# Kernel optimization log

Measured on AMD Instinct MI355X. Metric: run time of the kernel, lower is better.

The kernel has to match this reference:

```python
import jax, jax.numpy as jnp
import numpy as np
import math

SIGMA_DATA = 0.5
SIGMA_MIN = 0.002
SIGMA_MAX = 80.0
B = 32768
STATE = 256
ACT = 64
TD = 16
E = 16
H = 256  # moe hidden = gate_dim = output_dim = hidden_dim//4
IN = STATE + ACT + TD  # 336
TOP_K = 4


def mish(x):
    return x * jnp.tanh(jax.nn.softplus(x))


def setup_inputs() -> dict:
    key = jax.random.key(0)
    ks = jax.random.split(key, 20)
    def xavier(k, shape):
        fan_in, fan_out = shape[-2], shape[-1]
        lim = math.sqrt(6.0 / (fan_in + fan_out))
        return jax.random.uniform(k, shape, jnp.float32, -lim, lim)
    inp = {
        "x": jax.random.normal(ks[0], (B, ACT), jnp.float32),
        "sigma": jax.random.uniform(ks[1], (B,), jnp.float32) * (SIGMA_MAX - SIGMA_MIN) + SIGMA_MIN,
        "state": jax.random.normal(ks[2], (B, STATE), jnp.float32),
        # time MLP: Linear(16,32), Mish, Linear(32,16)
        "tW1": xavier(ks[3], (TD, 2 * TD)), "tb1": jnp.zeros((2 * TD,), jnp.float32),
        "tW2": xavier(ks[4], (2 * TD, TD)), "tb2": jnp.zeros((TD,), jnp.float32),
        # gate: Linear(IN, H), ReLU, (dropout eval), Linear(H, E)
        "gW1": xavier(ks[5], (IN, H)), "gb1": jnp.zeros((H,), jnp.float32),
        "gW2": xavier(ks[6], (H, E)), "gb2": jnp.zeros((E,), jnp.float32),
        # 16 stacked expert MLPs: IN->H->H->H with Mish after each Linear
        "eW1": xavier(ks[7], (E, IN, H)), "eb1": jnp.zeros((E, H), jnp.float32),
        "eW2": xavier(ks[8], (E, H, H)), "eb2": jnp.zeros((E, H), jnp.float32),
        "eW3": xavier(ks[9], (E, H, H)), "eb3": jnp.zeros((E, H), jnp.float32),
        # final layer: Linear(H, ACT)
        "fW": xavier(ks[10], (H, ACT)), "fb": jnp.zeros((ACT,), jnp.float32),
    }
    return inp


def reference(x, sigma, state, tW1, tb1, tW2, tb2, gW1, gb1, gW2, gb2,
              eW1, eb1, eW2, eb2, eW3, eb3, fW, fb):
    # --- consistency-model scalings (boundary condition) ---
    c_skip = SIGMA_DATA ** 2 / ((sigma - SIGMA_MIN) ** 2 + SIGMA_DATA ** 2)
    c_out = (sigma - SIGMA_MIN) * SIGMA_DATA * jax.lax.rsqrt(sigma ** 2 + SIGMA_DATA ** 2)
    c_in = jax.lax.rsqrt(sigma ** 2 + SIGMA_DATA ** 2)
    rescaled_t = 1000.0 * 0.25 * jnp.log(sigma + 1e-44)

    x_in = c_in[:, None] * x

    # --- sinusoidal time embedding (dim=16) + time MLP ---
    half = TD // 2
    freqs = jnp.exp(jnp.arange(half, dtype=jnp.float32) * (-math.log(10000.0) / (half - 1)))
    ang = rescaled_t[:, None] * freqs[None, :]           # [B, 8]
    pe = jnp.concatenate([jnp.sin(ang), jnp.cos(ang)], axis=-1)  # [B, 16]
    t = mish(pe @ tW1 + tb1) @ tW2 + tb2                 # [B, 16]

    inp = jnp.concatenate([x_in, t, state], axis=1)      # [B, 336]

    # --- gate (eval mode: dropout off) ---
    g = jax.nn.relu(inp @ gW1 + gb1) @ gW2 + gb2         # [B, E]
    gate_scores = jax.nn.softmax(g, axis=1)
    top_k_scores, top_k_idx = jax.lax.top_k(gate_scores, TOP_K)  # [B, K]

    # --- run ALL experts densely (as the original does) ---
    h = mish(jnp.einsum('bi,eih->beh', inp, eW1) + eb1)  # [B, E, H]
    h = mish(jnp.einsum('beh,ehk->bek', h, eW2) + eb2)
    expert_out = mish(jnp.einsum('beh,eho->beo', h, eW3) + eb3)  # [B, E, H]

    # --- gather top-k, scale by normalized gate scores, combine ---
    sel = jnp.take_along_axis(expert_out, top_k_idx[:, :, None], axis=1)  # [B, K, H]
    scaled = sel * top_k_scores[:, :, None]
    scaled = scaled / (jnp.sum(top_k_scores, axis=1, keepdims=True)[:, :, None] + 1e-9)
    combined = jnp.sum(scaled, axis=1)                   # [B, H]

    # --- auxiliary loss ---
    one_hot = jax.nn.one_hot(top_k_idx, E, dtype=jnp.float32)  # [B, K, E]
    expert_load = jnp.sum(one_hot, axis=(0, 1)) / (x.shape[0] + 1e-9)
    load_balancing_loss = jnp.var(expert_load, ddof=1)   # torch .var() is unbiased
    entropy = -jnp.mean(jnp.sum(gate_scores * jnp.log(gate_scores + 1e-9), axis=1))
    aux_loss = load_balancing_loss + entropy

    model_out = combined @ fW + fb                       # [B, ACT]
    denoised = c_out[:, None] * model_out + c_skip[:, None] * x
    denoised = jnp.clip(denoised, -1.0, 1.0)             # clip_denoised=True
    return denoised, aux_loss
```

## Files before the change

### kernel.cpp

```cpp
#include <hip/hip_runtime.h>
#include <math.h>

#define BN 32768
#define INDP 352
#define HD 256
#define AD 64
#define EN 16
#define TME 32
#define TMG 16
#define STOT (BN * 4)
#define GRID_E 4112
#define CHUNK_E 514

typedef __attribute__((ext_vector_type(8))) short s8v;
typedef __attribute__((ext_vector_type(4))) float f4v;
typedef unsigned short u16;

__device__ __forceinline__ u16 f2bf(float x) {
  unsigned u = __float_as_uint(x);
  return (u16)((u + 0x7fffu + ((u >> 16) & 1u)) >> 16);
}
__device__ __forceinline__ float bf2f(u16 h) { return __uint_as_float(((unsigned)h) << 16); }
__device__ __forceinline__ float rcpf(float a) { float r; asm("v_rcp_f32 %0, %1" : "=v"(r) : "v"(a)); return r; }
__device__ __forceinline__ float mishf(float x) {
  float xc = fminf(x, 30.f);
  float u = __expf(xc);
  float w = fmaf(u, u, u + u);
  return x * w * rcpf(w + 2.f);
}
__device__ __forceinline__ f4v mfma16(s8v a, s8v b, f4v c) {
  return __builtin_amdgcn_mfma_f32_16x16x32_bf16(a, b, c, 0, 0, 0);
}
__device__ __forceinline__ void pack8(const u16* q, u16* d) {
  uint4 u;
  u.x = q[0] | ((unsigned)q[1] << 16); u.y = q[2] | ((unsigned)q[3] << 16);
  u.z = q[4] | ((unsigned)q[5] << 16); u.w = q[6] | ((unsigned)q[7] << 16);
  *(uint4*)d = u;
}

__global__ void k_init(int* __restrict__ counts, int* __restrict__ cursor,
                       float* __restrict__ ent) {
  int i = threadIdx.x;
  if (i < 16) { counts[i] = 0; cursor[i] = 0; }
  if (i == 16) *ent = 0.f;
}

__global__ void k_prep(const float* __restrict__ src, u16* __restrict__ dst,
                       int Ksrc, int Spad, int NT, int N,
                       long sStride, long dStride, int NP, int total) {
  int idx = blockIdx.x * 256 + threadIdx.x;
  if (idx >= total) return;
  int l = idx & 63;
  int t = idx >> 6;
  int nt = t % NT; t /= NT;
  int s = t % Spad; t /= Spad;
  int m = t;
  const float* sp = src + (size_t)m * sStride;
  int n = nt * 16 + (l & 15);
  int kb = s * 32 + (l >> 4) * 8;
  u16 q0[8], q1[8], q2[8];
  #pragma unroll
  for (int i = 0; i < 8; ++i) {
    int k = kb + i;
    float v = (k < Ksrc) ? sp[(size_t)k * N + n] : 0.f;
    u16 a = f2bf(v); float r1 = v - bf2f(a);
    u16 b = f2bf(r1); float r2 = r1 - bf2f(b);
    q0[i] = a; q1[i] = b; q2[i] = f2bf(r2);
  }
  u16* d = dst + (size_t)m * dStride + (size_t)((s * NT + nt) * NP) * 512 + l * 8;
  pack8(q0, d);
  pack8(q1, d + 512);
  if (NP == 3) pack8(q2, d + 1024);
}

__global__ void k_time_inp(const float* __restrict__ x, const float* __restrict__ sigma,
                           const float* __restrict__ state,
                           const float* __restrict__ tW1, const float* __restrict__ tb1,
                           const float* __restrict__ tW2, const float* __restrict__ tb2,
                           u16* __restrict__ p0, u16* __restrict__ p1, u16* __restrict__ p2) {
  const int wv = threadIdx.x >> 6;
  const int lane = threadIdx.x & 63;
  const int row = blockIdx.x * 4 + wv;
  const float sg = sigma[row];
  const float rt = 250.0f * logf(sg + 1e-44f);
  float pe = 0.f;
  if (lane < 16) {
    int j = lane & 7;
    float f = expf(-1.3157629102823121f * (float)j);
    float ang = rt * f;
    pe = (lane < 8) ? sinf(ang) : cosf(ang);
  }
  float h1;
  {
    float acc = 0.f;
    int j = lane & 31;
    #pragma unroll
    for (int i = 0; i < 16; ++i) {
      float p = __shfl(pe, i, 64);
      acc = fmaf(p, tW1[i * 32 + j], acc);
    }
    acc += tb1[j];
    float sp = log1pf(expf(acc));
    h1 = acc * tanhf(sp);
  }
  float t2;
  {
    float acc = 0.f;
    int j = lane & 15;
    #pragma unroll
    for (int i = 0; i < 32; ++i) {
      float h = __shfl(h1, i, 64);
      acc = fmaf(h, tW2[i * 16 + j], acc);
    }
    t2 = acc + tb2[j];
  }
  const float c_in = rsqrtf(sg * sg + 0.25f);
  u16* r0 = p0 + (size_t)row * INDP;
  u16* r1 = p1 + (size_t)row * INDP;
  u16* r2 = p2 + (size_t)row * INDP;
  auto wsplit = [&](int c, float v) {
    u16 a = f2bf(v); float ra = v - bf2f(a);
    u16 b = f2bf(ra); float rb = ra - bf2f(b);
    r0[c] = a; r1[c] = b; r2[c] = f2bf(rb);
  };
  wsplit(lane, c_in * x[row * 64 + lane]);
  if (lane < 16) wsplit(64 + lane, t2);
  #pragma unroll
  for (int r = 0; r < 4; ++r)
    wsplit(80 + r * 64 + lane, state[(size_t)row * 256 + r * 64 + lane]);
  if (lane < 16) { r0[336 + lane] = 0; r1[336 + lane] = 0; r2[336 + lane] = 0; }
}

__global__ __launch_bounds__(256, 4) void k_gate(
    const u16* __restrict__ p0, const u16* __restrict__ p1, const u16* __restrict__ p2,
    const u16* __restrict__ gW1b, const float* __restrict__ gb1,
    const u16* __restrict__ gW2b, const float* __restrict__ gb2,
    int* __restrict__ topk_idx, float* __restrict__ topk_w,
    int* __restrict__ counts, float* __restrict__ ent_sum) {
  __shared__ __align__(16) u16 sH0[TMG * 256];
  __shared__ __align__(16) u16 sH1[TMG * 256];
  __shared__ __align__(16) u16 sH2[TMG * 256];
  __shared__ float sLog[TMG * 16];
  __shared__ int scnt[16];
  const int tid = threadIdx.x;
  const int l = tid & 63, wn = tid >> 6;
  const int g = l >> 4, r16 = l & 15;
  const int row0 = blockIdx.x * TMG;
  const int swz = (r16 & 7) << 3;
  if (tid < 16) scnt[tid] = 0;

  f4v acc[4];
  #pragma unroll
  for (int j = 0; j < 4; ++j) acc[j] = (f4v){0.f, 0.f, 0.f, 0.f};

  #pragma unroll
  for (int s = 0; s < 11; ++s) {
    s8v a0, a1, a2, b0[4], b1[4], b2[4];
    {
      size_t off = (size_t)(row0 + r16) * INDP + s * 32 + g * 8;
      a0 = *(const s8v*)(p0 + off);
      a1 = *(const s8v*)(p1 + off);
      a2 = *(const s8v*)(p2 + off);
    }
    #pragma unroll
    for (int j = 0; j < 4; ++j) {
      const u16* pb = gW1b + (size_t)((s * 16 + wn * 4 + j) * 3) * 512 + l * 8;
      b0[j] = *(const s8v*)pb;
      b1[j] = *(const s8v*)(pb + 512);
      b2[j] = *(const s8v*)(pb + 1024);
    }
    #pragma unroll
    for (int j = 0; j < 4; ++j) acc[j] = mfma16(a0, b0[j], acc[j]);
    #pragma unroll
    for (int j = 0; j < 4; ++j) acc[j] = mfma16(a0, b1[j], acc[j]);
    #pragma unroll
    for (int j = 0; j < 4; ++j) acc[j] = mfma16(a1, b0[j], acc[j]);
    #pragma unroll
    for (int j = 0; j < 4; ++j) acc[j] = mfma16(a1, b1[j], acc[j]);
    #pragma unroll
    for (int j = 0; j < 4; ++j) acc[j] = mfma16(a0, b2[j], acc[j]);
    #pragma unroll
    for (int j = 0; j < 4; ++j) acc[j] = mfma16(a2, b0[j], acc[j]);
  }
  #pragma unroll
  for (int j = 0; j < 4; ++j) {
    float bj = gb1[wn * 64 + j * 16 + r16];
    #pragma unroll
    for (int r = 0; r < 4; ++r) {
      int row = g * 4 + r;
      int col = wn * 64 + j * 16 + r16;
      float v = fmaxf(acc[j][r] + bj, 0.f);
      u16 h0 = f2bf(v); float ra = v - bf2f(h0);
      u16 h1 = f2bf(ra); float rb = ra - bf2f(h1);
      int ec = col ^ ((row & 7) << 3);
      sH0[row * 256 + ec] = h0;
      sH1[row * 256 + ec] = h1;
      sH2[row * 256 + ec] = f2bf(rb);
    }
  }
  __syncthreads();

  f4v l2 = (f4v){0.f, 0.f, 0.f, 0.f};
  #pragma unroll
  for (int s = 0; s < 8; ++s) {
    const u16* pb = gW2b + (size_t)(s * 3) * 512 + l * 8;
    s8v b0 = *(const s8v*)pb;
    s8v b1 = *(const s8v*)(pb + 512);
    s8v b2 = *(const s8v*)(pb + 1024);
    int ec = (s * 32 + g * 8) ^ swz;
    s8v a0 = *(const s8v*)&sH0[r16 * 256 + ec];
    s8v a1 = *(const s8v*)&sH1[r16 * 256 + ec];
    s8v a2 = *(const s8v*)&sH2[r16 * 256 + ec];
    l2 = mfma16(a0, b0, l2);
    l2 = mfma16(a0, b1, l2);
    l2 = mfma16(a1, b0, l2);
    l2 = mfma16(a1, b1, l2);
    l2 = mfma16(a0, b2, l2);
    l2 = mfma16(a2, b0, l2);
  }
  if (wn == 0) {
    #pragma unroll
    for (int r = 0; r < 4; ++r)
      sLog[(g * 4 + r) * 16 + r16] = l2[r] + gb2[r16];
  }
  __syncthreads();

  float entc = 0.f;
  if (tid < TMG) {
    const int row = row0 + tid;
    float gx[16], mx = -1e30f;
    #pragma unroll
    for (int e = 0; e < 16; ++e) { gx[e] = sLog[tid * 16 + e]; mx = fmaxf(mx, gx[e]); }
    float p[16], s = 0.f;
    #pragma unroll
    for (int e = 0; e < 16; ++e) { p[e] = expf(gx[e] - mx); s += p[e]; }
    const float inv = 1.f / s;
    #pragma unroll
    for (int e = 0; e < 16; ++e) {
      float pr = p[e] * inv;
      entc -= pr * logf(pr + 1e-9f);
    }
    int idxs[4]; float scs[4];
    unsigned used = 0;
    float wsum = 1e-9f;
    #pragma unroll
    for (int k = 0; k < 4; ++k) {
      int be = 0; float bv = -1.f;
      #pragma unroll
      for (int e = 0; e < 16; ++e) {
        float pr = p[e] * inv;
        if (!((used >> e) & 1u) && pr > bv) { bv = pr; be = e; }
      }
      used |= (1u << be);
      idxs[k] = be; scs[k] = bv;
      wsum += bv;
    }
    #pragma unroll
    for (int k = 0; k < 4; ++k) {
      topk_idx[row * 4 + k] = idxs[k];
      topk_w[row * 4 + k] = scs[k] / wsum;
      atomicAdd(&scnt[idxs[k]], 1);
    }
  }
  if (tid < 64) {
    #pragma unroll
    for (int off = 32; off > 0; off >>= 1) entc += __shfl_down(entc, off, 64);
  }
  if (tid == 0) atomicAdd(ent_sum, entc);
  __syncthreads();
  if (tid < 16 && scnt[tid] > 0) atomicAdd(&counts[tid], scnt[tid]);
}

__global__ void k_aux(const int* __restrict__ counts, const float* __restrict__ ent_sum,
                      int* __restrict__ offsets, int* __restrict__ tbk,
                      float* __restrict__ aux_out) {
  if (threadIdx.x == 0) {
    int off = 0, t = 0;
    float load[16], mean = 0.f;
    for (int e = 0; e < 16; ++e) {
      offsets[e] = off; tbk[e] = t;
      int c = counts[e];
      off += c;
      t += (c + TME - 1) / TME;
      load[e] = (float)c / (32768.0f + 1e-9f);
      mean += load[e];
    }
    offsets[16] = off; tbk[16] = t;
    mean *= (1.f / 16.f);
    float var = 0.f;
    for (int e = 0; e < 16; ++e) { float d = load[e] - mean; var += d * d; }
    var *= (1.f / 15.f);
    *aux_out = var + ent_sum[0] * (1.0f / 32768.0f);
  }
}

__global__ void k_scatter(const int* __restrict__ topk_idx, const float* __restrict__ topk_w,
                          const int* __restrict__ offsets, int* __restrict__ cursor,
                          int* __restrict__ slot_row, int* __restrict__ rslot) {
  __shared__ int cnt[16];
  __shared__ int base[16];
  const int tid = threadIdx.x;
  if (tid < 16) cnt[tid] = 0;
  __syncthreads();
  const int row = blockIdx.x * 256 + tid;
  int e4[4]; int lp[4];
  #pragma unroll
  for (int k = 0; k < 4; ++k) {
    e4[k] = topk_idx[row * 4 + k];
    lp[k] = atomicAdd(&cnt[e4[k]], 1);
  }
  __syncthreads();
  if (tid < 16) base[tid] = atomicAdd(&cursor[tid], cnt[tid]);
  __syncthreads();
  #pragma unroll
  for (int k = 0; k < 4; ++k) {
    int s = offsets[e4[k]] + base[e4[k]] + lp[k];
    slot_row[s] = row;
    rslot[row * 4 + k] = s;
  }
}

__global__ __launch_bounds__(256, 4) void k_expert(
    const u16* __restrict__ inpHi, const u16* __restrict__ inpLo,
    const u16* __restrict__ eW1b, const float* __restrict__ eb1,
    const u16* __restrict__ eW2b, const float* __restrict__ eb2,
    const u16* __restrict__ eW3b, const float* __restrict__ eb3,
    const u16* __restrict__ fWb,
    const int* __restrict__ offsets, const int* __restrict__ counts,
    const int* __restrict__ tbk, const int* __restrict__ slot_row,
    float* __restrict__ eout) {
  __shared__ __align__(16) u16 sHi[TME * 256];
  __shared__ __align__(16) u16 sLo[TME * 256];
  __shared__ int sRows[TME];

  const int bid = (blockIdx.x & 7) * CHUNK_E + (blockIdx.x >> 3);
  if (bid >= tbk[16]) return;
  int e = 0;
  #pragma unroll
  for (int i = 1; i < 16; ++i)
    if (bid >= tbk[i]) e = i;
  const int tile = bid - tbk[e];
  const int cnt = counts[e];
  const int s0 = offsets[e] + tile * TME;
  const int nr = min(TME, cnt - tile * TME);
  const int tid = threadIdx.x;
  const int l = tid & 63;
  const int wn = tid >> 6;
  const int g = l >> 4, r16 = l & 15;
  const int swz = (r16 & 7) << 3;

  if (tid < TME)
    sRows[tid] = (tid < nr) ? slot_row[s0 + tid] : slot_row[s0];
  __syncthreads();

  size_t rbase[2];
  #pragma unroll
  for (int mt = 0; mt < 2; ++mt)
    rbase[mt] = (size_t)sRows[mt * 16 + r16] * INDP;

  f4v acc[2][4];
  #pragma unroll
  for (int i = 0; i < 2; ++i)
    #pragma unroll
    for (int j = 0; j < 4; ++j) acc[i][j] = (f4v){0.f, 0.f, 0.f, 0.f};

  const u16* W1 = eW1b + (size_t)e * 180224;
  #pragma unroll
  for (int s = 0; s < 11; ++s) {
    s8v ah[2], al[2], bh[4], bl[4];
    #pragma unroll
    for (int mt = 0; mt < 2; ++mt) {
      size_t off = rbase[mt] + s * 32 + g * 8;
      ah[mt] = *(const s8v*)(inpHi + off);
      al[mt] = *(const s8v*)(inpLo + off);
    }
    #pragma unroll
    for (int j = 0; j < 4; ++j) {
      const u16* pb = W1 + (size_t)((s * 16 + wn * 4 + j) * 2) * 512 + l * 8;
      bh[j] = *(const s8v*)pb;
      bl[j] = *(const s8v*)(pb + 512);
    }
    #pragma unroll
    for (int mt = 0; mt < 2; ++mt)
      #pragma unroll
      for (int j = 0; j < 4; ++j) acc[mt][j] = mfma16(ah[mt], bh[j], acc[mt][j]);
    #pragma unroll
    for (int mt = 0; mt < 2; ++mt)
      #pragma unroll
      for (int j = 0; j < 4; ++j) acc[mt][j] = mfma16(al[mt], bh[j], acc[mt][j]);
    #pragma unroll
    for (int mt = 0; mt < 2; ++mt)
      #pragma unroll
      for (int j = 0; j < 4; ++j) acc[mt][j] = mfma16(ah[mt], bl[j], acc[mt][j]);
  }
  {
    const float* b1 = eb1 + e * HD;
    #pragma unroll
    for (int mt = 0; mt < 2; ++mt)
      #pragma unroll
      for (int j = 0; j < 4; ++j) {
        float bj = b1[wn * 64 + j * 16 + r16];
        #pragma unroll
        for (int r = 0; r < 4; ++r) {
          int row = mt * 16 + g * 4 + r;
          int col = wn * 64 + j * 16 + r16;
          float v = mishf(acc[mt][j][r] + bj);
          u16 h = f2bf(v);
          int ec = col ^ ((row & 7) << 3);
          sHi[row * 256 + ec] = h;
          sLo[row * 256 + ec] = f2bf(v - bf2f(h));
        }
      }
  }
  __syncthreads();

  #pragma unroll 1
  for (int L = 0; L < 2; ++L) {
    const u16* Wb = (L == 0 ? eW2b : eW3b) + (size_t)e * 131072;
    const float* bb = (L == 0 ? eb2 : eb3) + e * HD;
    f4v a2[2][4];
    #pragma unroll
    for (int i = 0; i < 2; ++i)
      #pragma unroll
      for (int j = 0; j < 4; ++j) a2[i][j] = (f4v){0.f, 0.f, 0.f, 0.f};
    #pragma unroll
    for (int s = 0; s < 8; ++s) {
      s8v ah[2], al[2], bh[4], bl[4];
      #pragma unroll
      for (int mt = 0; mt < 2; ++mt) {
        int row = mt * 16 + r16;
        int ec = (s * 32 + g * 8) ^ swz;
        ah[mt] = *(const s8v*)&sHi[row * 256 + ec];
        al[mt] = *(const s8v*)&sLo[row * 256 + ec];
      }
      #pragma unroll
      for (int j = 0; j < 4; ++j) {
        const u16* pb = Wb + (size_t)((s * 16 + wn * 4 + j) * 2) * 512 + l * 8;
        bh[j] = *(const s8v*)pb;
        bl[j] = *(const s8v*)(pb + 512);
      }
      #pragma unroll
      for (int mt = 0; mt < 2; ++mt)
        #pragma unroll
        for (int j = 0; j < 4; ++j) a2[mt][j] = mfma16(ah[mt], bh[j], a2[mt][j]);
      #pragma unroll
      for (int mt = 0; mt < 2; ++mt)
        #pragma unroll
        for (int j = 0; j < 4; ++j) a2[mt][j] = mfma16(al[mt], bh[j], a2[mt][j]);
      #pragma unroll
      for (int mt = 0; mt < 2; ++mt)
        #pragma unroll
        for (int j = 0; j < 4; ++j) a2[mt][j] = mfma16(ah[mt], bl[j], a2[mt][j]);
    }
    __syncthreads();
    #pragma unroll
    for (int mt = 0; mt < 2; ++mt)
      #pragma unroll
      for (int j = 0; j < 4; ++j) {
        float bj = bb[wn * 64 + j * 16 + r16];
        #pragma unroll
        for (int r = 0; r < 4; ++r) {
          int row = mt * 16 + g * 4 + r;
          int col = wn * 64 + j * 16 + r16;
          float v = mishf(a2[mt][j][r] + bj);
          u16 h = f2bf(v);
          int ec = col ^ ((row & 7) << 3);
          sHi[row * 256 + ec] = h;
          sLo[row * 256 + ec] = f2bf(v - bf2f(h));
        }
      }
    __syncthreads();
  }

  f4v a3[2];
  a3[0] = (f4v){0.f, 0.f, 0.f, 0.f};
  a3[1] = (f4v){0.f, 0.f, 0.f, 0.f};
  #pragma unroll
  for (int s = 0; s < 8; ++s) {
    s8v ah[2], al[2];
    #pragma unroll
    for (int mt = 0; mt < 2; ++mt) {
      int row = mt * 16 + r16;
      int ec = (s * 32 + g * 8) ^ swz;
      ah[mt] = *(const s8v*)&sHi[row * 256 + ec];
      al[mt] = *(const s8v*)&sLo[row * 256 + ec];
    }
    const u16* pb = fWb + (size_t)((s * 4 + wn) * 2) * 512 + l * 8;
    s8v bh = *(const s8v*)pb;
    s8v bl = *(const s8v*)(pb + 512);
    #pragma unroll
    for (int mt = 0; mt < 2; ++mt) {
      a3[mt] = mfma16(ah[mt], bh, a3[mt]);
      a3[mt] = mfma16(al[mt], bh, a3[mt]);
      a3[mt] = mfma16(ah[mt], bl, a3[mt]);
    }
  }
  #pragma unroll
  for (int mt = 0; mt < 2; ++mt)
    #pragma unroll
    for (int r = 0; r < 4; ++r) {
      int rl = mt * 16 + g * 4 + r;
      if (rl < nr)
        eout[(size_t)(s0 + rl) * AD + wn * 16 + r16] = a3[mt][r];
    }
}

__global__ void k_final(const float* __restrict__ x, const float* __restrict__ sigma,
                        const float* __restrict__ fb, const int* __restrict__ rslot,
                        const float* __restrict__ topk_w, const float* __restrict__ eout,
                        float* __restrict__ out) {
  int i = blockIdx.x * 256 + threadIdx.x;
  if (i >= BN * AD) return;
  int row = i >> 6, c = i & 63;
  float a = 0.f;
  #pragma unroll
  for (int k = 0; k < 4; ++k)
    a = fmaf(topk_w[row * 4 + k], eout[(size_t)rslot[row * 4 + k] * AD + c], a);
  float sg = sigma[row];
  float sm = sg - 0.002f;
  float c_skip = 0.25f / (sm * sm + 0.25f);
  float c_out = sm * 0.5f * rsqrtf(sg * sg + 0.25f);
  float d = c_out * (a + fb[c]) + c_skip * x[i];
  out[i] = fminf(fmaxf(d, -1.f), 1.f);
}

extern "C" void kernel_launch(void* const* d_in, const int* in_sizes, int n_in,
                              void* d_out, int out_size, void* d_ws, size_t ws_size,
                              hipStream_t stream) {
  const float* x     = (const float*)d_in[0];
  const float* sigma = (const float*)d_in[1];
  const float* state = (const float*)d_in[2];
  const float* tW1   = (const float*)d_in[3];
  const float* tb1   = (const float*)d_in[4];
  const float* tW2   = (const float*)d_in[5];
  const float* tb2   = (const float*)d_in[6];
  const float* gW1   = (const float*)d_in[7];
  const float* gb1   = (const float*)d_in[8];
  const float* gW2   = (const float*)d_in[9];
  const float* gb2   = (const float*)d_in[10];
  const float* eW1   = (const float*)d_in[11];
  const float* eb1   = (const float*)d_in[12];
  const float* eW2   = (const float*)d_in[13];
  const float* eb2   = (const float*)d_in[14];
  const float* eW3   = (const float*)d_in[15];
  const float* eb3   = (const float*)d_in[16];
  const float* fW    = (const float*)d_in[17];
  const float* fb    = (const float*)d_in[18];
  float* out = (float*)d_out;

  char* p = (char*)d_ws;
  auto alloc = [&](size_t bytes) { void* r = (void*)p; p += (bytes + 255) & ~(size_t)255; return r; };
  u16* inpHi  = (u16*)alloc((size_t)BN * INDP * 2);
  u16* inpLo  = (u16*)alloc((size_t)BN * INDP * 2);
  u16* inpMid = (u16*)alloc((size_t)BN * INDP * 2);
  u16* gW1b   = (u16*)alloc((size_t)11 * 16 * 3 * 512 * 2);
  u16* gW2b   = (u16*)alloc((size_t)8 * 3 * 512 * 2);
  u16* eW1b   = (u16*)alloc((size_t)16 * 180224 * 2);
  u16* eW2b   = (u16*)alloc((size_t)16 * 131072 * 2);
  u16* eW3b   = (u16*)alloc((size_t)16 * 131072 * 2);
  u16* fWb    = (u16*)alloc((size_t)32768 * 2);
  float* eout = (float*)alloc((size_t)STOT * AD * 4);
  int*   topk_idx = (int*)alloc((size_t)BN * 4 * 4);
  float* topk_w   = (float*)alloc((size_t)BN * 4 * 4);
  int*   rslot    = (int*)alloc((size_t)BN * 4 * 4);
  int*   counts   = (int*)alloc(64);
  int*   cursor   = (int*)alloc(64);
  int*   offsets  = (int*)alloc(68);
  int*   tbk      = (int*)alloc(68);
  float* ent      = (float*)alloc(4);
  int*   slot_row = (int*)alloc((size_t)STOT * 4);

  k_init<<<1, 64, 0, stream>>>(counts, cursor, ent);

  int tot;
  tot = 16 * 11 * 16 * 64;
  k_prep<<<(tot + 255) / 256, 256, 0, stream>>>(eW1, eW1b, 336, 11, 16, 256,
                                                (long)336 * 256, 180224, 2, tot);
  tot = 16 * 8 * 16 * 64;
  k_prep<<<(tot + 255) / 256, 256, 0, stream>>>(eW2, eW2b, 256, 8, 16, 256,
                                                (long)256 * 256, 131072, 2, tot);
  k_prep<<<(tot + 255) / 256, 256, 0, stream>>>(eW3, eW3b, 256, 8, 16, 256,
                                                (long)256 * 256, 131072, 2, tot);
  tot = 11 * 16 * 64;
  k_prep<<<(tot + 255) / 256, 256, 0, stream>>>(gW1, gW1b, 336, 11, 16, 256,
                                                0, 0, 3, tot);
  tot = 8 * 1 * 64;
  k_prep<<<(tot + 255) / 256, 256, 0, stream>>>(gW2, gW2b, 256, 8, 1, 16,
                                                0, 0, 3, tot);
  tot = 8 * 4 * 64;
  k_prep<<<(tot + 255) / 256, 256, 0, stream>>>(fW, fWb, 256, 8, 4, 64,
                                                0, 0, 2, tot);

  k_time_inp<<<BN / 4, 256, 0, stream>>>(x, sigma, state, tW1, tb1, tW2, tb2,
                                         inpHi, inpLo, inpMid);
  k_gate<<<BN / TMG, 256, 0, stream>>>(inpHi, inpLo, inpMid, gW1b, gb1, gW2b, gb2,
                                       topk_idx, topk_w, counts, ent);
  k_aux<<<1, 64, 0, stream>>>(counts, ent, offsets, tbk, out + (size_t)BN * AD);
  k_scatter<<<BN / 256, 256, 0, stream>>>(topk_idx, topk_w, offsets, cursor,
                                          slot_row, rslot);
  k_expert<<<GRID_E, 256, 0, stream>>>(inpHi, inpLo, eW1b, eb1, eW2b, eb2,
                                       eW3b, eb3, fWb, offsets, counts, tbk,
                                       slot_row, eout);
  k_final<<<(BN * AD + 255) / 256, 256, 0, stream>>>(x, sigma, fb, rslot,
                                                     topk_w, eout, out);
}
```

Measured before the change: 531.6 us.

## Fuse prep kernels, software-pipeline expert GEMMs, and atomically combine expert outputs

```diff
diff --git a/kernel.cpp b/kernel.cpp
--- a/kernel.cpp
+++ b/kernel.cpp
@@ -38,21 +38,59 @@
   *(uint4*)d = u;
 }
 
-__global__ void k_init(int* __restrict__ counts, int* __restrict__ cursor,
-                       float* __restrict__ ent) {
-  int i = threadIdx.x;
-  if (i < 16) { counts[i] = 0; cursor[i] = 0; }
-  if (i == 16) *ent = 0.f;
-}
-
-__global__ void k_prep(const float* __restrict__ src, u16* __restrict__ dst,
-                       int Ksrc, int Spad, int NT, int N,
-                       long sStride, long dStride, int NP, int total) {
-  int idx = blockIdx.x * 256 + threadIdx.x;
-  if (idx >= total) return;
+__device__ __forceinline__ void ldB4(const u16* __restrict__ W, int s, int wn, int l,
+                                     s8v (&bh)[4], s8v (&bl)[4]) {
+  #pragma unroll
+  for (int j = 0; j < 4; ++j) {
+    const u16* pb = W + (size_t)((s * 16 + wn * 4 + j) * 2) * 512 + l * 8;
+    bh[j] = *(const s8v*)pb;
+    bl[j] = *(const s8v*)(pb + 512);
+  }
+}
+__device__ __forceinline__ void ldA1(const u16* __restrict__ pHi, const u16* __restrict__ pLo,
+                                     const size_t (&rbase)[2], int s, int g,
+                                     s8v (&ah)[2], s8v (&al)[2]) {
+  #pragma unroll
+  for (int mt = 0; mt < 2; ++mt) {
+    size_t off = rbase[mt] + s * 32 + g * 8;
+    ah[mt] = *(const s8v*)(pHi + off);
+    al[mt] = *(const s8v*)(pLo + off);
+  }
+}
+__device__ __forceinline__ void ldA2(const u16* __restrict__ sHi, const u16* __restrict__ sLo,
+                                     int s, int g, int r16, int swz,
+                                     s8v (&ah)[2], s8v (&al)[2]) {
+  int ec = (s * 32 + g * 8) ^ swz;
+  #pragma unroll
+  for (int mt = 0; mt < 2; ++mt) {
+    int row = mt * 16 + r16;
+    ah[mt] = *(const s8v*)&sHi[row * 256 + ec];
+    al[mt] = *(const s8v*)&sLo[row * 256 + ec];
+  }
+}
+__device__ __forceinline__ void fmas24(f4v (&acc)[2][4], const s8v (&ah)[2], const s8v (&al)[2],
+                                       const s8v (&bh)[4], const s8v (&bl)[4]) {
+  #pragma unroll
+  for (int mt = 0; mt < 2; ++mt)
+    #pragma unroll
+    for (int j = 0; j < 4; ++j) acc[mt][j] = mfma16(ah[mt], bh[j], acc[mt][j]);
+  #pragma unroll
+  for (int mt = 0; mt < 2; ++mt)
+    #pragma unroll
+    for (int j = 0; j < 4; ++j) acc[mt][j] = mfma16(al[mt], bh[j], acc[mt][j]);
+  #pragma unroll
+  for (int mt = 0; mt < 2; ++mt)
+    #pragma unroll
+    for (int j = 0; j < 4; ++j) acc[mt][j] = mfma16(ah[mt], bl[j], acc[mt][j]);
+}
+
+__device__ __forceinline__ void prep_seg(const float* __restrict__ src, u16* __restrict__ dst,
+                                         int Ksrc, int NT, int N,
+                                         long sStride, long dStride, int NP, int idx) {
   int l = idx & 63;
   int t = idx >> 6;
   int nt = t % NT; t /= NT;
+  int Spad = (Ksrc + 31) / 32;
   int s = t % Spad; t /= Spad;
   int m = t;
   const float* sp = src + (size_t)m * sStride;
@@ -73,11 +111,38 @@
   if (NP == 3) pack8(q2, d + 1024);
 }
 
+__global__ void k_prep_all(const float* __restrict__ eW1, const float* __restrict__ eW2,
+                           const float* __restrict__ eW3, const float* __restrict__ gW1,
+                           const float* __restrict__ gW2, const float* __restrict__ fW,
+                           u16* __restrict__ eW1b, u16* __restrict__ eW2b,
+                           u16* __restrict__ eW3b, u16* __restrict__ gW1b,
+                           u16* __restrict__ gW2b, u16* __restrict__ fWb,
+                           int* __restrict__ counts, int* __restrict__ cursor,
+                           float* __restrict__ ent) {
+  int idx = blockIdx.x * 256 + threadIdx.x;
+  if (idx < 180224) { prep_seg(eW1, eW1b, 336, 16, 256, (long)336 * 256, 180224, 2, idx); return; }
+  idx -= 180224;
+  if (idx < 131072) { prep_seg(eW2, eW2b, 256, 16, 256, (long)256 * 256, 131072, 2, idx); return; }
+  idx -= 131072;
+  if (idx < 131072) { prep_seg(eW3, eW3b, 256, 16, 256, (long)256 * 256, 131072, 2, idx); return; }
+  idx -= 131072;
+  if (idx < 11264) { prep_seg(gW1, gW1b, 336, 16, 256, 0, 0, 3, idx); return; }
+  idx -= 11264;
+  if (idx < 512) { prep_seg(gW2, gW2b, 256, 1, 16, 0, 0, 3, idx); return; }
+  idx -= 512;
+  if (idx < 2048) { prep_seg(fW, fWb, 256, 4, 64, 0, 0, 2, idx); return; }
+  idx -= 2048;
+  if (idx < 16) { counts[idx] = 0; cursor[idx] = 0; }
+  if (idx == 16) *ent = 0.f;
+}
+
 __global__ void k_time_inp(const float* __restrict__ x, const float* __restrict__ sigma,
                            const float* __restrict__ state,
                            const float* __restrict__ tW1, const float* __restrict__ tb1,
                            const float* __restrict__ tW2, const float* __restrict__ tb2,
-                           u16* __restrict__ p0, u16* __restrict__ p1, u16* __restrict__ p2) {
+                           u16* __restrict__ p0, u16* __restrict__ p1, u16* __restrict__ p2,
+                           float* __restrict__ out) {
+  out[blockIdx.x * 256 + threadIdx.x] = 0.f;
   const int wv = threadIdx.x >> 6;
   const int lane = threadIdx.x & 63;
   const int row = blockIdx.x * 4 + wv;
@@ -296,17 +361,18 @@
 
 __global__ void k_scatter(const int* __restrict__ topk_idx, const float* __restrict__ topk_w,
                           const int* __restrict__ offsets, int* __restrict__ cursor,
-                          int* __restrict__ slot_row, int* __restrict__ rslot) {
+                          int* __restrict__ slot_row, float* __restrict__ slot_w) {
   __shared__ int cnt[16];
   __shared__ int base[16];
   const int tid = threadIdx.x;
   if (tid < 16) cnt[tid] = 0;
   __syncthreads();
   const int row = blockIdx.x * 256 + tid;
-  int e4[4]; int lp[4];
+  int e4[4]; float w4[4]; int lp[4];
   #pragma unroll
   for (int k = 0; k < 4; ++k) {
     e4[k] = topk_idx[row * 4 + k];
+    w4[k] = topk_w[row * 4 + k];
     lp[k] = atomicAdd(&cnt[e4[k]], 1);
   }
   __syncthreads();
@@ -316,11 +382,11 @@
   for (int k = 0; k < 4; ++k) {
     int s = offsets[e4[k]] + base[e4[k]] + lp[k];
     slot_row[s] = row;
-    rslot[row * 4 + k] = s;
-  }
-}
-
-__global__ __launch_bounds__(256, 4) void k_expert(
+    slot_w[s] = w4[k];
+  }
+}
+
+__global__ __launch_bounds__(256, 3) void k_expert(
     const u16* __restrict__ inpHi, const u16* __restrict__ inpLo,
     const u16* __restrict__ eW1b, const float* __restrict__ eb1,
     const u16* __restrict__ eW2b, const float* __restrict__ eb2,
@@ -328,10 +394,11 @@
     const u16* __restrict__ fWb,
     const int* __restrict__ offsets, const int* __restrict__ counts,
     const int* __restrict__ tbk, const int* __restrict__ slot_row,
-    float* __restrict__ eout) {
+    const float* __restrict__ slot_w, float* __restrict__ out) {
   __shared__ __align__(16) u16 sHi[TME * 256];
   __shared__ __align__(16) u16 sLo[TME * 256];
   __shared__ int sRows[TME];
+  __shared__ float sWv[TME];
 
   const int bid = (blockIdx.x & 7) * CHUNK_E + (blockIdx.x >> 3);
   if (bid >= tbk[16]) return;
@@ -349,14 +416,15 @@
   const int g = l >> 4, r16 = l & 15;
   const int swz = (r16 & 7) << 3;
 
-  if (tid < TME)
+  if (tid < TME) {
     sRows[tid] = (tid < nr) ? slot_row[s0 + tid] : slot_row[s0];
+    sWv[tid] = (tid < nr) ? slot_w[s0 + tid] : 0.f;
+  }
   __syncthreads();
 
   size_t rbase[2];
-  #pragma unroll
-  for (int mt = 0; mt < 2; ++mt)
-    rbase[mt] = (size_t)sRows[mt * 16 + r16] * INDP;
+  rbase[0] = (size_t)sRows[r16] * INDP;
+  rbase[1] = (size_t)sRows[16 + r16] * INDP;
 
   f4v acc[2][4];
   #pragma unroll
@@ -365,33 +433,21 @@
     for (int j = 0; j < 4; ++j) acc[i][j] = (f4v){0.f, 0.f, 0.f, 0.f};
 
   const u16* W1 = eW1b + (size_t)e * 180224;
-  #pragma unroll
-  for (int s = 0; s < 11; ++s) {
-    s8v ah[2], al[2], bh[4], bl[4];
-    #pragma unroll
-    for (int mt = 0; mt < 2; ++mt) {
-      size_t off = rbase[mt] + s * 32 + g * 8;
-      ah[mt] = *(const s8v*)(inpHi + off);
-      al[mt] = *(const s8v*)(inpLo + off);
-    }
-    #pragma unroll
-    for (int j = 0; j < 4; ++j) {
-      const u16* pb = W1 + (size_t)((s * 16 + wn * 4 + j) * 2) * 512 + l * 8;
-      bh[j] = *(const s8v*)pb;
-      bl[j] = *(const s8v*)(pb + 512);
-    }
-    #pragma unroll
-    for (int mt = 0; mt < 2; ++mt)
-      #pragma unroll
-      for (int j = 0; j < 4; ++j) acc[mt][j] = mfma16(ah[mt], bh[j], acc[mt][j]);
-    #pragma unroll
-    for (int mt = 0; mt < 2; ++mt)
-      #pragma unroll
-      for (int j = 0; j < 4; ++j) acc[mt][j] = mfma16(al[mt], bh[j], acc[mt][j]);
-    #pragma unroll
-    for (int mt = 0; mt < 2; ++mt)
-      #pragma unroll
-      for (int j = 0; j < 4; ++j) acc[mt][j] = mfma16(ah[mt], bl[j], acc[mt][j]);
+  {
+    s8v ahA[2], alA[2], bhA[4], blA[4];
+    s8v ahB[2], alB[2], bhB[4], blB[4];
+    ldA1(inpHi, inpLo, rbase, 0, g, ahA, alA);
+    ldB4(W1, 0, wn, l, bhA, blA);
+    #pragma unroll
+    for (int s2 = 0; s2 < 5; ++s2) {
+      ldA1(inpHi, inpLo, rbase, 2 * s2 + 1, g, ahB, alB);
+      ldB4(W1, 2 * s2 + 1, wn, l, bhB, blB);
+      fmas24(acc, ahA, alA, bhA, blA);
+      ldA1(inpHi, inpLo, rbase, 2 * s2 + 2, g, ahA, alA);
+      ldB4(W1, 2 * s2 + 2, wn, l, bhA, blA);
+      fmas24(acc, ahB, alB, bhB, blB);
+    }
+    fmas24(acc, ahA, alA, bhA, blA);
   }
   {
     const float* b1 = eb1 + e * HD;
@@ -423,34 +479,22 @@
     for (int i = 0; i < 2; ++i)
       #pragma unroll
       for (int j = 0; j < 4; ++j) a2[i][j] = (f4v){0.f, 0.f, 0.f, 0.f};
-    #pragma unroll
-    for (int s = 0; s < 8; ++s) {
-      s8v ah[2], al[2], bh[4], bl[4];
+    {
+      s8v ahA[2], alA[2], bhA[4], blA[4];
+      s8v ahB[2], alB[2], bhB[4], blB[4];
+      ldA2(sHi, sLo, 0, g, r16, swz, ahA, alA);
+      ldB4(Wb, 0, wn, l, bhA, blA);
       #pragma unroll
-      for (int mt = 0; mt < 2; ++mt) {
-        int row = mt * 16 + r16;
-        int ec = (s * 32 + g * 8) ^ swz;
-        ah[mt] = *(const s8v*)&sHi[row * 256 + ec];
-        al[mt] = *(const s8v*)&sLo[row * 256 + ec];
+      for (int s2 = 0; s2 < 4; ++s2) {
+        ldA2(sHi, sLo, 2 * s2 + 1, g, r16, swz, ahB, alB);
+        ldB4(Wb, 2 * s2 + 1, wn, l, bhB, blB);
+        fmas24(a2, ahA, alA, bhA, blA);
+        if (s2 < 3) {
+          ldA2(sHi, sLo, 2 * s2 + 2, g, r16, swz, ahA, alA);
+          ldB4(Wb, 2 * s2 + 2, wn, l, bhA, blA);
+        }
+        fmas24(a2, ahB, alB, bhB, blB);
       }
-      #pragma unroll
-      for (int j = 0; j < 4; ++j) {
-        const u16* pb = Wb + (size_t)((s * 16 + wn * 4 + j) * 2) * 512 + l * 8;
-        bh[j] = *(const s8v*)pb;
-        bl[j] = *(const s8v*)(pb + 512);
-      }
-      #pragma unroll
-      for (int mt = 0; mt < 2; ++mt)
-        #pragma unroll
-        for (int j = 0; j < 4; ++j) a2[mt][j] = mfma16(ah[mt], bh[j], a2[mt][j]);
-      #pragma unroll
-      for (int mt = 0; mt < 2; ++mt)
-        #pragma unroll
-        for (int j = 0; j < 4; ++j) a2[mt][j] = mfma16(al[mt], bh[j], a2[mt][j]);
-      #pragma unroll
-      for (int mt = 0; mt < 2; ++mt)
-        #pragma unroll
-        for (int j = 0; j < 4; ++j) a2[mt][j] = mfma16(ah[mt], bl[j], a2[mt][j]);
     }
     __syncthreads();
     #pragma unroll
@@ -475,24 +519,34 @@
   f4v a3[2];
   a3[0] = (f4v){0.f, 0.f, 0.f, 0.f};
   a3[1] = (f4v){0.f, 0.f, 0.f, 0.f};
-  #pragma unroll
-  for (int s = 0; s < 8; ++s) {
-    s8v ah[2], al[2];
-    #pragma unroll
-    for (int mt = 0; mt < 2; ++mt) {
-      int row = mt * 16 + r16;
-      int ec = (s * 32 + g * 8) ^ swz;
-      ah[mt] = *(const s8v*)&sHi[row * 256 + ec];
-      al[mt] = *(const s8v*)&sLo[row * 256 + ec];
-    }
-    const u16* pb = fWb + (size_t)((s * 4 + wn) * 2) * 512 + l * 8;
-    s8v bh = *(const s8v*)pb;
-    s8v bl = *(const s8v*)(pb + 512);
-    #pragma unroll
-    for (int mt = 0; mt < 2; ++mt) {
-      a3[mt] = mfma16(ah[mt], bh, a3[mt]);
-      a3[mt] = mfma16(al[mt], bh, a3[mt]);
-      a3[mt] = mfma16(ah[mt], bl, a3[mt]);
+  {
+    s8v ahA[2], alA[2], ahB[2], alB[2];
+    s8v bhA, blA, bhB, blB;
+    auto ldBF = [&](int s, s8v& bh, s8v& bl) {
+      const u16* pb = fWb + (size_t)((s * 4 + wn) * 2) * 512 + l * 8;
+      bh = *(const s8v*)pb;
+      bl = *(const s8v*)(pb + 512);
+    };
+    auto fmas6 = [&](const s8v (&ah)[2], const s8v (&al)[2], s8v bh, s8v bl) {
+      a3[0] = mfma16(ah[0], bh, a3[0]);
+      a3[1] = mfma16(ah[1], bh, a3[1]);
+      a3[0] = mfma16(al[0], bh, a3[0]);
+      a3[1] = mfma16(al[1], bh, a3[1]);
+      a3[0] = mfma16(ah[0], bl, a3[0]);
+      a3[1] = mfma16(ah[1], bl, a3[1]);
+    };
+    ldA2(sHi, sLo, 0, g, r16, swz, ahA, alA);
+    ldBF(0, bhA, blA);
+    #pragma unroll
+    for (int s2 = 0; s2 < 4; ++s2) {
+      ldA2(sHi, sLo, 2 * s2 + 1, g, r16, swz, ahB, alB);
+      ldBF(2 * s2 + 1, bhB, blB);
+      fmas6(ahA, alA, bhA, blA);
+      if (s2 < 3) {
+        ldA2(sHi, sLo, 2 * s2 + 2, g, r16, swz, ahA, alA);
+        ldBF(2 * s2 + 2, bhA, blA);
+      }
+      fmas6(ahB, alB, bhB, blB);
     }
   }
   #pragma unroll
@@ -500,27 +554,23 @@
     #pragma unroll
     for (int r = 0; r < 4; ++r) {
       int rl = mt * 16 + g * 4 + r;
-      if (rl < nr)
-        eout[(size_t)(s0 + rl) * AD + wn * 16 + r16] = a3[mt][r];
+      if (rl < nr) {
+        float v = a3[mt][r] * sWv[rl];
+        atomicAdd(&out[(size_t)sRows[rl] * AD + wn * 16 + r16], v);
+      }
     }
 }
 
 __global__ void k_final(const float* __restrict__ x, const float* __restrict__ sigma,
-                        const float* __restrict__ fb, const int* __restrict__ rslot,
-                        const float* __restrict__ topk_w, const float* __restrict__ eout,
-                        float* __restrict__ out) {
+                        const float* __restrict__ fb, float* __restrict__ out) {
   int i = blockIdx.x * 256 + threadIdx.x;
   if (i >= BN * AD) return;
   int row = i >> 6, c = i & 63;
-  float a = 0.f;
-  #pragma unroll
-  for (int k = 0; k < 4; ++k)
-    a = fmaf(topk_w[row * 4 + k], eout[(size_t)rslot[row * 4 + k] * AD + c], a);
   float sg = sigma[row];
   float sm = sg - 0.002f;
   float c_skip = 0.25f / (sm * sm + 0.25f);
   float c_out = sm * 0.5f * rsqrtf(sg * sg + 0.25f);
-  float d = c_out * (a + fb[c]) + c_skip * x[i];
+  float d = c_out * (out[i] + fb[c]) + c_skip * x[i];
   out[i] = fminf(fmaxf(d, -1.f), 1.f);
 }
 
@@ -559,48 +609,28 @@
   u16* eW2b   = (u16*)alloc((size_t)16 * 131072 * 2);
   u16* eW3b   = (u16*)alloc((size_t)16 * 131072 * 2);
   u16* fWb    = (u16*)alloc((size_t)32768 * 2);
-  float* eout = (float*)alloc((size_t)STOT * AD * 4);
   int*   topk_idx = (int*)alloc((size_t)BN * 4 * 4);
   float* topk_w   = (float*)alloc((size_t)BN * 4 * 4);
-  int*   rslot    = (int*)alloc((size_t)BN * 4 * 4);
   int*   counts   = (int*)alloc(64);
   int*   cursor   = (int*)alloc(64);
   int*   offsets  = (int*)alloc(68);
   int*   tbk      = (int*)alloc(68);
   float* ent      = (float*)alloc(4);
   int*   slot_row = (int*)alloc((size_t)STOT * 4);
-
-  k_init<<<1, 64, 0, stream>>>(counts, cursor, ent);
-
-  int tot;
-  tot = 16 * 11 * 16 * 64;
-  k_prep<<<(tot + 255) / 256, 256, 0, stream>>>(eW1, eW1b, 336, 11, 16, 256,
-                                                (long)336 * 256, 180224, 2, tot);
-  tot = 16 * 8 * 16 * 64;
-  k_prep<<<(tot + 255) / 256, 256, 0, stream>>>(eW2, eW2b, 256, 8, 16, 256,
-                                                (long)256 * 256, 131072, 2, tot);
-  k_prep<<<(tot + 255) / 256, 256, 0, stream>>>(eW3, eW3b, 256, 8, 16, 256,
-                                                (long)256 * 256, 131072, 2, tot);
-  tot = 11 * 16 * 64;
-  k_prep<<<(tot + 255) / 256, 256, 0, stream>>>(gW1, gW1b, 336, 11, 16, 256,
-                                                0, 0, 3, tot);
-  tot = 8 * 1 * 64;
-  k_prep<<<(tot + 255) / 256, 256, 0, stream>>>(gW2, gW2b, 256, 8, 1, 16,
-                                                0, 0, 3, tot);
-  tot = 8 * 4 * 64;
-  k_prep<<<(tot + 255) / 256, 256, 0, stream>>>(fW, fWb, 256, 8, 4, 64,
-                                                0, 0, 2, tot);
-
+  float* slot_w   = (float*)alloc((size_t)STOT * 4);
+
+  k_prep_all<<<1783, 256, 0, stream>>>(eW1, eW2, eW3, gW1, gW2, fW,
+                                       eW1b, eW2b, eW3b, gW1b, gW2b, fWb,
+                                       counts, cursor, ent);
   k_time_inp<<<BN / 4, 256, 0, stream>>>(x, sigma, state, tW1, tb1, tW2, tb2,
-                                         inpHi, inpLo, inpMid);
+                                         inpHi, inpLo, inpMid, out);
   k_gate<<<BN / TMG, 256, 0, stream>>>(inpHi, inpLo, inpMid, gW1b, gb1, gW2b, gb2,
                                        topk_idx, topk_w, counts, ent);
   k_aux<<<1, 64, 0, stream>>>(counts, ent, offsets, tbk, out + (size_t)BN * AD);
   k_scatter<<<BN / 256, 256, 0, stream>>>(topk_idx, topk_w, offsets, cursor,
-                                          slot_row, rslot);
+                                          slot_row, slot_w);
   k_expert<<<GRID_E, 256, 0, stream>>>(inpHi, inpLo, eW1b, eb1, eW2b, eb2,
                                        eW3b, eb3, fWb, offsets, counts, tbk,
-                                       slot_row, eout);
-  k_final<<<(BN * AD + 255) / 256, 256, 0, stream>>>(x, sigma, fb, rslot,
-                                                     topk_w, eout, out);
-}
+                                       slot_row, slot_w, out);
+  k_final<<<(BN * AD + 255) / 256, 256, 0, stream>>>(x, sigma, fb, out);
+}
```

Measured after the change: 503.1 us. 5.4% less time.
